# Performance work log

Hardware: AMD Instinct MI355X
Metric: run time of the kernel (lower is better)

The kernel has to match this reference:

```python
import jax, jax.numpy as jnp
import numpy as np

B, S, D, E, K = 4, 4096, 2048, 64, 8
STD = 0.02 / np.sqrt(D)
BIAS_UPDATE_SPEED = 0.001


def setup_inputs() -> dict:
    key = jax.random.key(0)
    k1, k2, k3, k4 = jax.random.split(key, 4)
    return {
        "x": jax.random.normal(k1, (B, S, D), dtype=jnp.float32),
        "Wr": (jax.random.normal(k2, (E, D), dtype=jnp.float32) * STD),
        "Wn": (jax.random.normal(k3, (E, D), dtype=jnp.float32) * STD),
        "bias": jnp.zeros((E,), dtype=jnp.float32),
        "noise_u": jax.random.uniform(k4, (B, S, E), dtype=jnp.float32),
    }


def reference(x, Wr, Wn, bias, noise_u):
    # x: [B,S,D]; Wr, Wn: [E,D]; bias: [E]; noise_u: [B,S,E] uniform(0,1)
    logits = jnp.einsum("bsd,ed->bse", x, Wr)          # router logits
    noisy_logits = jnp.einsum("bsd,ed->bse", x, Wn)    # noise scale logits
    noise = noise_u * jax.nn.softplus(noisy_logits)
    z = noise + logits + bias                           # [B,S,E]

    topk_vals, topk_idx = jax.lax.top_k(z, K)           # [B,S,K]
    neg_inf = jnp.full_like(z, -jnp.inf)
    sparse = jnp.put_along_axis(neg_inf, topk_idx, topk_vals, axis=-1,
                                inplace=False)          # -inf except top-k slots
    probs = jax.nn.softmax(sparse, axis=-1)             # [B,S,E]

    # load-balancing bias update (faithful to source, incl. scalar sum quirk)
    sel_mask = jax.nn.one_hot(topk_idx, E, dtype=jnp.float32).sum(axis=(0, 1, 2))  # [E]
    current_expert_load = sel_mask.sum()                # scalar (as in torch .sum(0) on 1-D)
    total_tokens = B * S * K
    avg_load = total_tokens / E
    load_violation = avg_load - current_expert_load
    new_bias = bias + BIAS_UPDATE_SPEED * jnp.sign(load_violation)

    return probs, topk_idx, new_bias
```

## Files before the change

kernel.cpp:

```cpp
#include <hip/hip_runtime.h>
#include <math.h>

#define BB 4
#define SS 4096
#define DD 2048
#define EE 64
#define KK 8
#define TT_TOTAL (BB*SS)
#define E2 128
#define DK 32
#define NC (DD/DK)

typedef double double2_t __attribute__((ext_vector_type(2)));
typedef double double4_t __attribute__((ext_vector_type(4)));

__device__ __forceinline__ double softplus64(double x) {
    return fmax(x, 0.0) + log1p(exp(-fabs(x)));
}

#define ROWF 132

template<int KS>
__launch_bounds__(256, 2)
__global__ void gemmf_kernel(const float* __restrict__ x,
                             const float* __restrict__ Wr,
                             const float* __restrict__ Wn,
                             double* __restrict__ zp)
{
    __shared__ __align__(16) float xs[DK][ROWF];
    __shared__ __align__(16) float ws[DK][ROWF];

    const int tid   = threadIdx.x;
    const int split = blockIdx.x % KS;
    const int bt    = blockIdx.x / KS;
    const int tok0  = bt * 128;
    const int kbase = split * (DD / KS);
    const int NCH   = (DD / KS) / DK;

    const int srow = tid & 127;
    const int skh  = tid >> 7;
    const float* xsrc = x + (size_t)(tok0 + srow) * DD + kbase + 16 * skh;
    const float* wsrc = ((srow < EE) ? Wr + (size_t)srow * DD
                                     : Wn + (size_t)(srow - EE) * DD)
                        + kbase + 16 * skh;

    const int og2 = tid & 15;
    const int tg2 = tid >> 4;

    double acc[8][8];
    #pragma unroll
    for (int t = 0; t < 8; ++t)
        #pragma unroll
        for (int o = 0; o < 8; ++o) acc[t][o] = 0.0;

    float4 xa[4], wa[4];
    #pragma unroll
    for (int i = 0; i < 4; ++i) {
        xa[i] = *reinterpret_cast<const float4*>(xsrc + 4 * i);
        wa[i] = *reinterpret_cast<const float4*>(wsrc + 4 * i);
    }

    for (int c = 0; c < NCH; ++c) {
        __syncthreads();

        {
            const int k0 = 16 * skh;
            #pragma unroll
            for (int i = 0; i < 4; ++i) {
                xs[k0 + 4*i + 0][srow] = xa[i].x;
                xs[k0 + 4*i + 1][srow] = xa[i].y;
                xs[k0 + 4*i + 2][srow] = xa[i].z;
                xs[k0 + 4*i + 3][srow] = xa[i].w;
                ws[k0 + 4*i + 0][srow] = wa[i].x;
                ws[k0 + 4*i + 1][srow] = wa[i].y;
                ws[k0 + 4*i + 2][srow] = wa[i].z;
                ws[k0 + 4*i + 3][srow] = wa[i].w;
            }
        }
        __syncthreads();

        if (c + 1 < NCH) {
            const int off = (c + 1) * DK;
            #pragma unroll
            for (int i = 0; i < 4; ++i) {
                xa[i] = *reinterpret_cast<const float4*>(xsrc + off + 4 * i);
                wa[i] = *reinterpret_cast<const float4*>(wsrc + off + 4 * i);
            }
        }

        #pragma unroll 4
        for (int k = 0; k < DK; ++k) {
            const float4 fx0 = *reinterpret_cast<const float4*>(&xs[k][4 * tg2]);
            const float4 fx1 = *reinterpret_cast<const float4*>(&xs[k][64 + 4 * tg2]);
            const float4 fw0 = *reinterpret_cast<const float4*>(&ws[k][4 * og2]);
            const float4 fw1 = *reinterpret_cast<const float4*>(&ws[k][64 + 4 * og2]);
            const double xv[8] = {(double)fx0.x, (double)fx0.y, (double)fx0.z, (double)fx0.w,
                                  (double)fx1.x, (double)fx1.y, (double)fx1.z, (double)fx1.w};
            const double wv[8] = {(double)fw0.x, (double)fw0.y, (double)fw0.z, (double)fw0.w,
                                  (double)fw1.x, (double)fw1.y, (double)fw1.z, (double)fw1.w};
            #pragma unroll
            for (int t = 0; t < 8; ++t)
                #pragma unroll
                for (int o = 0; o < 8; ++o)
                    acc[t][o] = fma(xv[t], wv[o], acc[t][o]);
        }
    }

    double* zbase = zp + (size_t)split * TT_TOTAL * E2;
    #pragma unroll
    for (int t = 0; t < 8; ++t) {
        const int tok = 4 * tg2 + (t & 3) + 64 * (t >> 2);
        double* row = zbase + (size_t)(tok0 + tok) * E2;
        double2_t v0 = {acc[t][0], acc[t][1]};
        double2_t v1 = {acc[t][2], acc[t][3]};
        double2_t v2 = {acc[t][4], acc[t][5]};
        double2_t v3 = {acc[t][6], acc[t][7]};
        *reinterpret_cast<double2_t*>(&row[4 * og2])          = v0;
        *reinterpret_cast<double2_t*>(&row[4 * og2 + 2])      = v1;
        *reinterpret_cast<double2_t*>(&row[64 + 4 * og2])     = v2;
        *reinterpret_cast<double2_t*>(&row[64 + 4 * og2 + 2]) = v3;
    }
}

template<int KS>
__launch_bounds__(256, 4)
__global__ void topk2_kernel(const double* __restrict__ zp,
                             const float* __restrict__ bias,
                             const float* __restrict__ noise_u,
                             float* __restrict__ out_probs,
                             float* __restrict__ out_idx)
{
    const int tid  = threadIdx.x;
    const int wid  = tid >> 6;
    const int lane = tid & 63;
    const int tok0 = blockIdx.x * 32;

    for (int tt = 0; tt < 8; ++tt) {
        const int tok = tok0 + wid * 8 + tt;
        const size_t gtok = (size_t)tok;

        double logit = 0.0, noisy = 0.0;
        #pragma unroll
        for (int s = 0; s < KS; ++s) {
            const double* row = zp + (size_t)s * TT_TOTAL * E2 + (size_t)tok * E2;
            logit += row[lane];
            noisy += row[EE + lane];
        }
        const double zv = (double)noise_u[gtok * EE + lane] * softplus64(noisy)
                          + logit + (double)bias[lane];

        double zw = zv;
        bool   sel = false;
        double m0  = 0.0;
        #pragma unroll
        for (int it = 0; it < KK; ++it) {
            double v  = zw;
            int    ix = lane;
            #pragma unroll
            for (int off = 32; off > 0; off >>= 1) {
                const double ov = __shfl_xor(v, off, 64);
                const int    oi = __shfl_xor(ix, off, 64);
                if (ov > v || (ov == v && oi < ix)) { v = ov; ix = oi; }
            }
            if (it == 0) m0 = v;
            if (lane == ix) { sel = true; zw = -INFINITY; }
            if (lane == 0) out_idx[gtok * KK + it] = (float)ix;
        }

        const double ex = sel ? exp(zv - m0) : 0.0;
        double den = ex;
        #pragma unroll
        for (int off = 32; off > 0; off >>= 1) den += __shfl_xor(den, off, 64);

        out_probs[gtok * EE + lane] = (float)(ex / den);
    }
}

#define BT 32
#define XT 34
#define WT 66

__launch_bounds__(256, 4)
__global__ void gemm_kernel(const float* __restrict__ x,
                            const float* __restrict__ Wr,
                            const float* __restrict__ Wn,
                            double* __restrict__ zout)
{
    __shared__ __align__(16) double xs[DK][XT];
    __shared__ __align__(16) double ws[DK][WT];

    const int tid  = threadIdx.x;
    const int bt   = blockIdx.x >> 1;
    const int be   = blockIdx.x & 1;
    const int tok0 = bt * BT;
    const int e0   = be * 64;

    const int kk = tid & 31;
    const int tq = tid >> 5;
    const float* xsrc[4];
    const float* wsrc[8];
    #pragma unroll
    for (int j = 0; j < 4; ++j)
        xsrc[j] = x + (size_t)(tok0 + 4 * tq + j) * DD + kk;
    #pragma unroll
    for (int j = 0; j < 4; ++j) {
        const int e  = e0 + 4 * tq + j;
        const int e2 = e0 + 32 + 4 * tq + j;
        wsrc[j]     = ((e  < EE) ? Wr + (size_t)e * DD
                                 : Wn + (size_t)(e  - EE) * DD) + kk;
        wsrc[4 + j] = ((e2 < EE) ? Wr + (size_t)e2 * DD
                                 : Wn + (size_t)(e2 - EE) * DD) + kk;
    }

    const int og = tid & 15;
    const int tp = tid >> 4;

    double acc[2][4];
    #pragma unroll
    for (int t = 0; t < 2; ++t)
        #pragma unroll
        for (int i = 0; i < 4; ++i) acc[t][i] = 0.0;

    float xr[4], wr[8];
    #pragma unroll
    for (int j = 0; j < 4; ++j) xr[j] = xsrc[j][0];
    #pragma unroll
    for (int j = 0; j < 8; ++j) wr[j] = wsrc[j][0];

    for (int c = 0; c < NC; ++c) {
        __syncthreads();
        {
            double4_t xv = {(double)xr[0], (double)xr[1], (double)xr[2], (double)xr[3]};
            *reinterpret_cast<double4_t*>(&xs[kk][4 * tq]) = xv;
            double4_t w0 = {(double)wr[0], (double)wr[1], (double)wr[2], (double)wr[3]};
            *reinterpret_cast<double4_t*>(&ws[kk][4 * tq]) = w0;
            double4_t w1 = {(double)wr[4], (double)wr[5], (double)wr[6], (double)wr[7]};
            *reinterpret_cast<double4_t*>(&ws[kk][32 + 4 * tq]) = w1;
        }
        __syncthreads();
        if (c + 1 < NC) {
            const int off = (c + 1) * DK;
            #pragma unroll
            for (int j = 0; j < 4; ++j) xr[j] = xsrc[j][off];
            #pragma unroll
            for (int j = 0; j < 8; ++j) wr[j] = wsrc[j][off];
        }
        #pragma unroll 4
        for (int k = 0; k < DK; ++k) {
            const double2_t xv = *reinterpret_cast<const double2_t*>(&xs[k][2 * tp]);
            const double2_t w0 = *reinterpret_cast<const double2_t*>(&ws[k][2 * og]);
            const double2_t w1 = *reinterpret_cast<const double2_t*>(&ws[k][32 + 2 * og]);
            acc[0][0] = fma(xv.x, w0.x, acc[0][0]);
            acc[0][1] = fma(xv.x, w0.y, acc[0][1]);
            acc[0][2] = fma(xv.x, w1.x, acc[0][2]);
            acc[0][3] = fma(xv.x, w1.y, acc[0][3]);
            acc[1][0] = fma(xv.y, w0.x, acc[1][0]);
            acc[1][1] = fma(xv.y, w0.y, acc[1][1]);
            acc[1][2] = fma(xv.y, w1.x, acc[1][2]);
            acc[1][3] = fma(xv.y, w1.y, acc[1][3]);
        }
    }

    #pragma unroll
    for (int t = 0; t < 2; ++t) {
        const size_t base = (size_t)(tok0 + 2 * tp + t) * E2 + e0;
        double2_t lo = {acc[t][0], acc[t][1]};
        double2_t hi = {acc[t][2], acc[t][3]};
        *reinterpret_cast<double2_t*>(&zout[base + 2 * og])      = lo;
        *reinterpret_cast<double2_t*>(&zout[base + 32 + 2 * og]) = hi;
    }
}

#define F_XT 34
#define F_WR 130
#define F_ZR 130
#define F_SMEM ((DK*F_XT + DK*F_WR)*8)

__launch_bounds__(256, 3)
__global__ void router_kernel(const float* __restrict__ x,
                              const float* __restrict__ Wr,
                              const float* __restrict__ Wn,
                              const float* __restrict__ bias,
                              const float* __restrict__ noise_u,
                              float* __restrict__ out_probs,
                              float* __restrict__ out_idx)
{
    __shared__ __align__(16) char smem_raw[F_SMEM];
    double (*xs)[F_XT] = reinterpret_cast<double(*)[F_XT]>(smem_raw);
    double (*wt)[F_WR] = reinterpret_cast<double(*)[F_WR]>(smem_raw + DK*F_XT*8);
    double (*zbuf)[F_ZR] = reinterpret_cast<double(*)[F_ZR]>(smem_raw);

    const int tid  = threadIdx.x;
    const int tok0 = blockIdx.x * 32;
    const int stok = tid >> 3;
    const int sfi  = tid & 7;
    const float* xsrc = x + (size_t)(tok0 + stok) * DD + sfi * 4;
    const float* wsrc[4];
    #pragma unroll
    for (int it = 0; it < 4; ++it) {
        const int r = it * 32 + stok;
        wsrc[it] = ((r < EE) ? (Wr + (size_t)r * DD)
                             : (Wn + (size_t)(r - EE) * DD)) + sfi * 4;
    }
    const int tg = tid >> 5;
    const int eg = tid & 31;

    double acc[4][4];
    #pragma unroll
    for (int t = 0; t < 4; ++t)
        #pragma unroll
        for (int i = 0; i < 4; ++i) acc[t][i] = 0.0;

    float4 xr  = *reinterpret_cast<const float4*>(xsrc);
    float4 wr0 = *reinterpret_cast<const float4*>(wsrc[0]);
    float4 wr1 = *reinterpret_cast<const float4*>(wsrc[1]);
    float4 wr2 = *reinterpret_cast<const float4*>(wsrc[2]);
    float4 wr3 = *reinterpret_cast<const float4*>(wsrc[3]);

    for (int c = 0; c < NC; ++c) {
        __syncthreads();
        {
            const int k0 = sfi * 4;
            xs[k0+0][stok] = (double)xr.x;  xs[k0+1][stok] = (double)xr.y;
            xs[k0+2][stok] = (double)xr.z;  xs[k0+3][stok] = (double)xr.w;
            wt[k0+0][stok      ] = (double)wr0.x; wt[k0+1][stok      ] = (double)wr0.y;
            wt[k0+2][stok      ] = (double)wr0.z; wt[k0+3][stok      ] = (double)wr0.w;
            wt[k0+0][stok + 32 ] = (double)wr1.x; wt[k0+1][stok + 32 ] = (double)wr1.y;
            wt[k0+2][stok + 32 ] = (double)wr1.z; wt[k0+3][stok + 32 ] = (double)wr1.w;
            wt[k0+0][stok + 64 ] = (double)wr2.x; wt[k0+1][stok + 64 ] = (double)wr2.y;
            wt[k0+2][stok + 64 ] = (double)wr2.z; wt[k0+3][stok + 64 ] = (double)wr2.w;
            wt[k0+0][stok + 96 ] = (double)wr3.x; wt[k0+1][stok + 96 ] = (double)wr3.y;
            wt[k0+2][stok + 96 ] = (double)wr3.z; wt[k0+3][stok + 96 ] = (double)wr3.w;
        }
        __syncthreads();
        if (c + 1 < NC) {
            const int off = (c + 1) * DK;
            xr  = *reinterpret_cast<const float4*>(xsrc + off);
            wr0 = *reinterpret_cast<const float4*>(wsrc[0] + off);
            wr1 = *reinterpret_cast<const float4*>(wsrc[1] + off);
            wr2 = *reinterpret_cast<const float4*>(wsrc[2] + off);
            wr3 = *reinterpret_cast<const float4*>(wsrc[3] + off);
        }
        #pragma unroll 4
        for (int k = 0; k < DK; ++k) {
            const double2_t xv0 = *reinterpret_cast<const double2_t*>(&xs[k][tg * 4]);
            const double2_t xv1 = *reinterpret_cast<const double2_t*>(&xs[k][tg * 4 + 2]);
            const double2_t w0  = *reinterpret_cast<const double2_t*>(&wt[k][2 * eg]);
            const double2_t w1  = *reinterpret_cast<const double2_t*>(&wt[k][64 + 2 * eg]);
            const double xvv[4] = {xv0.x, xv0.y, xv1.x, xv1.y};
            #pragma unroll
            for (int t = 0; t < 4; ++t) {
                acc[t][0] = fma(xvv[t], w0.x, acc[t][0]);
                acc[t][1] = fma(xvv[t], w0.y, acc[t][1]);
                acc[t][2] = fma(xvv[t], w1.x, acc[t][2]);
                acc[t][3] = fma(xvv[t], w1.y, acc[t][3]);
            }
        }
    }
    __syncthreads();
    #pragma unroll
    for (int t = 0; t < 4; ++t) {
        double2_t lo = {acc[t][0], acc[t][1]};
        double2_t hi = {acc[t][2], acc[t][3]};
        *reinterpret_cast<double2_t*>(&zbuf[tg * 4 + t][2 * eg])      = lo;
        *reinterpret_cast<double2_t*>(&zbuf[tg * 4 + t][64 + 2 * eg]) = hi;
    }
    __syncthreads();

    const int wid  = tid >> 6;
    const int lane = tid & 63;
    for (int tt = 0; tt < 8; ++tt) {
        const int tok = wid * 8 + tt;
        const size_t gtok = (size_t)tok0 + tok;
        const double logit = zbuf[tok][lane];
        const double noisy = zbuf[tok][EE + lane];
        const double zv = (double)noise_u[gtok * EE + lane] * softplus64(noisy)
                          + logit + (double)bias[lane];
        double zw = zv;
        bool   sel = false;
        double m0  = 0.0;
        #pragma unroll
        for (int it = 0; it < KK; ++it) {
            double v  = zw;
            int    ix = lane;
            #pragma unroll
            for (int off = 32; off > 0; off >>= 1) {
                const double ov = __shfl_xor(v, off, 64);
                const int    oi = __shfl_xor(ix, off, 64);
                if (ov > v || (ov == v && oi < ix)) { v = ov; ix = oi; }
            }
            if (it == 0) m0 = v;
            if (lane == ix) { sel = true; zw = -INFINITY; }
            if (lane == 0) out_idx[gtok * KK + it] = (float)ix;
        }
        const double ex = sel ? exp(zv - m0) : 0.0;
        double den = ex;
        #pragma unroll
        for (int off = 32; off > 0; off >>= 1) den += __shfl_xor(den, off, 64);
        out_probs[gtok * EE + lane] = (float)(ex / den);
    }
}

__global__ void bias_kernel(const float* __restrict__ bias,
                            float* __restrict__ out_bias)
{
    const int e = threadIdx.x;
    if (e < EE) {
        const double load_violation = (double)(TT_TOTAL * KK) / EE
                                      - (double)(TT_TOTAL * KK);
        const double s = (load_violation > 0.0) ? 1.0
                         : ((load_violation < 0.0) ? -1.0 : 0.0);
        out_bias[e] = bias[e] + (float)(0.001 * s);
    }
}

extern "C" void kernel_launch(void* const* d_in, const int* in_sizes, int n_in,
                              void* d_out, int out_size, void* d_ws, size_t ws_size,
                              hipStream_t stream)
{
    const float* x       = (const float*)d_in[0];
    const float* Wr      = (const float*)d_in[1];
    const float* Wn      = (const float*)d_in[2];
    const float* bias    = (const float*)d_in[3];
    const float* noise_u = (const float*)d_in[4];

    float* out       = (float*)d_out;
    float* out_probs = out;
    float* out_idx   = out + (size_t)TT_TOTAL * EE;
    float* out_bias  = out + (size_t)TT_TOTAL * EE + (size_t)TT_TOTAL * KK;

    const size_t z1 = (size_t)TT_TOTAL * E2 * sizeof(double);

    if (ws_size >= 4 * z1) {
        double* zp = (double*)d_ws;
        gemmf_kernel<4><<<128 * 4, 256, 0, stream>>>(x, Wr, Wn, zp);
        topk2_kernel<4><<<TT_TOTAL / 32, 256, 0, stream>>>(zp, bias, noise_u,
                                                           out_probs, out_idx);
    } else if (ws_size >= 2 * z1) {
        double* zp = (double*)d_ws;
        gemmf_kernel<2><<<128 * 2, 256, 0, stream>>>(x, Wr, Wn, zp);
        topk2_kernel<2><<<TT_TOTAL / 32, 256, 0, stream>>>(zp, bias, noise_u,
                                                           out_probs, out_idx);
    } else if (ws_size >= z1) {
        double* z = (double*)d_ws;
        gemm_kernel<<<(TT_TOTAL / BT) * 2, 256, 0, stream>>>(x, Wr, Wn, z);
        topk2_kernel<1><<<TT_TOTAL / 32, 256, 0, stream>>>(z, bias, noise_u,
                                                           out_probs, out_idx);
    } else {
        router_kernel<<<TT_TOTAL / 32, 256, 0, stream>>>(
            x, Wr, Wn, bias, noise_u, out_probs, out_idx);
    }
    bias_kernel<<<1, 64, 0, stream>>>(bias, out_bias);
}
```

Before: 237.7 us.

## Compute router GEMM in fp32 with fp64 repair for near-tie tokens

Replaces the fp64 split-K GEMM with an fp32 version that writes fp32 partials, which halves workspace traffic and uses the much faster fp32 FMA path. The top-k kernel runs in fp32 and flags tokens whose gaps among the top-9 values fall below a small threshold. A repair kernel then recomputes those tokens in fp64 so the selected indices match the reference. Split-K can now go to 8 and occupancy rises to 4 blocks; the cost is an extra atomic flag list, a zero kernel and a repair pass, and correctness depends on the threshold being large enough.

```diff
diff --git a/kernel.cpp b/kernel.cpp
--- a/kernel.cpp
+++ b/kernel.cpp
@@ -10,22 +10,25 @@
 #define E2 128
 #define DK 32
 #define NC (DD/DK)
+#define DELTA 1e-4f
 
 typedef double double2_t __attribute__((ext_vector_type(2)));
-typedef double double4_t __attribute__((ext_vector_type(4)));
 
 __device__ __forceinline__ double softplus64(double x) {
     return fmax(x, 0.0) + log1p(exp(-fabs(x)));
 }
+__device__ __forceinline__ float softplus32(float x) {
+    return fmaxf(x, 0.0f) + log1pf(expf(-fabsf(x)));
+}
 
 #define ROWF 132
 
 template<int KS>
-__launch_bounds__(256, 2)
-__global__ void gemmf_kernel(const float* __restrict__ x,
-                             const float* __restrict__ Wr,
-                             const float* __restrict__ Wn,
-                             double* __restrict__ zp)
+__launch_bounds__(256, 4)
+__global__ void gemmf32_kernel(const float* __restrict__ x,
+                               const float* __restrict__ Wr,
+                               const float* __restrict__ Wn,
+                               float* __restrict__ zp)
 {
     __shared__ __align__(16) float xs[DK][ROWF];
     __shared__ __align__(16) float ws[DK][ROWF];
@@ -47,11 +50,11 @@
     const int og2 = tid & 15;
     const int tg2 = tid >> 4;
 
-    double acc[8][8];
+    float acc[8][8];
     #pragma unroll
     for (int t = 0; t < 8; ++t)
         #pragma unroll
-        for (int o = 0; o < 8; ++o) acc[t][o] = 0.0;
+        for (int o = 0; o < 8; ++o) acc[t][o] = 0.0f;
 
     float4 xa[4], wa[4];
     #pragma unroll
@@ -62,7 +65,6 @@
 
     for (int c = 0; c < NCH; ++c) {
         __syncthreads();
-
         {
             const int k0 = 16 * skh;
             #pragma unroll
@@ -94,41 +96,39 @@
             const float4 fx1 = *reinterpret_cast<const float4*>(&xs[k][64 + 4 * tg2]);
             const float4 fw0 = *reinterpret_cast<const float4*>(&ws[k][4 * og2]);
             const float4 fw1 = *reinterpret_cast<const float4*>(&ws[k][64 + 4 * og2]);
-            const double xv[8] = {(double)fx0.x, (double)fx0.y, (double)fx0.z, (double)fx0.w,
-                                  (double)fx1.x, (double)fx1.y, (double)fx1.z, (double)fx1.w};
-            const double wv[8] = {(double)fw0.x, (double)fw0.y, (double)fw0.z, (double)fw0.w,
-                                  (double)fw1.x, (double)fw1.y, (double)fw1.z, (double)fw1.w};
+            const float xv[8] = {fx0.x, fx0.y, fx0.z, fx0.w,
+                                 fx1.x, fx1.y, fx1.z, fx1.w};
+            const float wv[8] = {fw0.x, fw0.y, fw0.z, fw0.w,
+                                 fw1.x, fw1.y, fw1.z, fw1.w};
             #pragma unroll
             for (int t = 0; t < 8; ++t)
                 #pragma unroll
                 for (int o = 0; o < 8; ++o)
-                    acc[t][o] = fma(xv[t], wv[o], acc[t][o]);
-        }
-    }
-
-    double* zbase = zp + (size_t)split * TT_TOTAL * E2;
+                    acc[t][o] = fmaf(xv[t], wv[o], acc[t][o]);
+        }
+    }
+
+    float* zbase = zp + (size_t)split * TT_TOTAL * E2;
     #pragma unroll
     for (int t = 0; t < 8; ++t) {
         const int tok = 4 * tg2 + (t & 3) + 64 * (t >> 2);
-        double* row = zbase + (size_t)(tok0 + tok) * E2;
-        double2_t v0 = {acc[t][0], acc[t][1]};
-        double2_t v1 = {acc[t][2], acc[t][3]};
-        double2_t v2 = {acc[t][4], acc[t][5]};
-        double2_t v3 = {acc[t][6], acc[t][7]};
-        *reinterpret_cast<double2_t*>(&row[4 * og2])          = v0;
-        *reinterpret_cast<double2_t*>(&row[4 * og2 + 2])      = v1;
-        *reinterpret_cast<double2_t*>(&row[64 + 4 * og2])     = v2;
-        *reinterpret_cast<double2_t*>(&row[64 + 4 * og2 + 2]) = v3;
+        float* row = zbase + (size_t)(tok0 + tok) * E2;
+        float4 v0 = {acc[t][0], acc[t][1], acc[t][2], acc[t][3]};
+        float4 v1 = {acc[t][4], acc[t][5], acc[t][6], acc[t][7]};
+        *reinterpret_cast<float4*>(&row[4 * og2])      = v0;
+        *reinterpret_cast<float4*>(&row[64 + 4 * og2]) = v1;
     }
 }
 
 template<int KS>
 __launch_bounds__(256, 4)
-__global__ void topk2_kernel(const double* __restrict__ zp,
+__global__ void topkf_kernel(const float* __restrict__ zp,
                              const float* __restrict__ bias,
                              const float* __restrict__ noise_u,
                              float* __restrict__ out_probs,
-                             float* __restrict__ out_idx)
+                             float* __restrict__ out_idx,
+                             int* __restrict__ flag_list,
+                             int* __restrict__ flag_cnt)
 {
     const int tid  = threadIdx.x;
     const int wid  = tid >> 6;
@@ -139,135 +139,137 @@
         const int tok = tok0 + wid * 8 + tt;
         const size_t gtok = (size_t)tok;
 
-        double logit = 0.0, noisy = 0.0;
+        float logit = 0.0f, noisy = 0.0f;
         #pragma unroll
         for (int s = 0; s < KS; ++s) {
-            const double* row = zp + (size_t)s * TT_TOTAL * E2 + (size_t)tok * E2;
+            const float* row = zp + (size_t)s * TT_TOTAL * E2 + (size_t)tok * E2;
             logit += row[lane];
             noisy += row[EE + lane];
         }
-        const double zv = (double)noise_u[gtok * EE + lane] * softplus64(noisy)
-                          + logit + (double)bias[lane];
-
-        double zw = zv;
-        bool   sel = false;
-        double m0  = 0.0;
-        #pragma unroll
-        for (int it = 0; it < KK; ++it) {
-            double v  = zw;
-            int    ix = lane;
+        const float zv = noise_u[gtok * EE + lane] * softplus32(noisy)
+                         + logit + bias[lane];
+
+        float zw = zv;
+        bool  sel = false;
+        float vr[9];
+        #pragma unroll
+        for (int it = 0; it < 9; ++it) {
+            float v  = zw;
+            int   ix = lane;
             #pragma unroll
             for (int off = 32; off > 0; off >>= 1) {
-                const double ov = __shfl_xor(v, off, 64);
-                const int    oi = __shfl_xor(ix, off, 64);
+                const float ov = __shfl_xor(v, off, 64);
+                const int   oi = __shfl_xor(ix, off, 64);
                 if (ov > v || (ov == v && oi < ix)) { v = ov; ix = oi; }
             }
-            if (it == 0) m0 = v;
-            if (lane == ix) { sel = true; zw = -INFINITY; }
-            if (lane == 0) out_idx[gtok * KK + it] = (float)ix;
-        }
-
-        const double ex = sel ? exp(zv - m0) : 0.0;
-        double den = ex;
+            vr[it] = v;
+            if (it < 8) {
+                if (lane == ix) { sel = true; zw = -INFINITY; }
+                if (lane == 0) out_idx[gtok * KK + it] = (float)ix;
+            }
+        }
+
+        const float ex = sel ? expf(zv - vr[0]) : 0.0f;
+        float den = ex;
         #pragma unroll
         for (int off = 32; off > 0; off >>= 1) den += __shfl_xor(den, off, 64);
-
-        out_probs[gtok * EE + lane] = (float)(ex / den);
-    }
-}
-
-#define BT 32
-#define XT 34
-#define WT 66
+        out_probs[gtok * EE + lane] = ex / den;
+
+        if (lane == 0) {
+            float mg = vr[0] - vr[1];
+            #pragma unroll
+            for (int i = 1; i < 8; ++i) mg = fminf(mg, vr[i] - vr[i + 1]);
+            if (mg < DELTA) {
+                const int p = atomicAdd(flag_cnt, 1);
+                flag_list[p] = tok;
+            }
+        }
+    }
+}
 
 __launch_bounds__(256, 4)
-__global__ void gemm_kernel(const float* __restrict__ x,
-                            const float* __restrict__ Wr,
-                            const float* __restrict__ Wn,
-                            double* __restrict__ zout)
-{
-    __shared__ __align__(16) double xs[DK][XT];
-    __shared__ __align__(16) double ws[DK][WT];
-
-    const int tid  = threadIdx.x;
-    const int bt   = blockIdx.x >> 1;
-    const int be   = blockIdx.x & 1;
-    const int tok0 = bt * BT;
-    const int e0   = be * 64;
-
-    const int kk = tid & 31;
-    const int tq = tid >> 5;
-    const float* xsrc[4];
-    const float* wsrc[8];
-    #pragma unroll
-    for (int j = 0; j < 4; ++j)
-        xsrc[j] = x + (size_t)(tok0 + 4 * tq + j) * DD + kk;
-    #pragma unroll
-    for (int j = 0; j < 4; ++j) {
-        const int e  = e0 + 4 * tq + j;
-        const int e2 = e0 + 32 + 4 * tq + j;
-        wsrc[j]     = ((e  < EE) ? Wr + (size_t)e * DD
-                                 : Wn + (size_t)(e  - EE) * DD) + kk;
-        wsrc[4 + j] = ((e2 < EE) ? Wr + (size_t)e2 * DD
-                                 : Wn + (size_t)(e2 - EE) * DD) + kk;
-    }
-
-    const int og = tid & 15;
-    const int tp = tid >> 4;
-
-    double acc[2][4];
-    #pragma unroll
-    for (int t = 0; t < 2; ++t)
-        #pragma unroll
-        for (int i = 0; i < 4; ++i) acc[t][i] = 0.0;
-
-    float xr[4], wr[8];
-    #pragma unroll
-    for (int j = 0; j < 4; ++j) xr[j] = xsrc[j][0];
-    #pragma unroll
-    for (int j = 0; j < 8; ++j) wr[j] = wsrc[j][0];
-
-    for (int c = 0; c < NC; ++c) {
-        __syncthreads();
-        {
-            double4_t xv = {(double)xr[0], (double)xr[1], (double)xr[2], (double)xr[3]};
-            *reinterpret_cast<double4_t*>(&xs[kk][4 * tq]) = xv;
-            double4_t w0 = {(double)wr[0], (double)wr[1], (double)wr[2], (double)wr[3]};
-            *reinterpret_cast<double4_t*>(&ws[kk][4 * tq]) = w0;
-            double4_t w1 = {(double)wr[4], (double)wr[5], (double)wr[6], (double)wr[7]};
-            *reinterpret_cast<double4_t*>(&ws[kk][32 + 4 * tq]) = w1;
-        }
-        __syncthreads();
-        if (c + 1 < NC) {
-            const int off = (c + 1) * DK;
-            #pragma unroll
-            for (int j = 0; j < 4; ++j) xr[j] = xsrc[j][off];
-            #pragma unroll
-            for (int j = 0; j < 8; ++j) wr[j] = wsrc[j][off];
-        }
-        #pragma unroll 4
-        for (int k = 0; k < DK; ++k) {
-            const double2_t xv = *reinterpret_cast<const double2_t*>(&xs[k][2 * tp]);
-            const double2_t w0 = *reinterpret_cast<const double2_t*>(&ws[k][2 * og]);
-            const double2_t w1 = *reinterpret_cast<const double2_t*>(&ws[k][32 + 2 * og]);
-            acc[0][0] = fma(xv.x, w0.x, acc[0][0]);
-            acc[0][1] = fma(xv.x, w0.y, acc[0][1]);
-            acc[0][2] = fma(xv.x, w1.x, acc[0][2]);
-            acc[0][3] = fma(xv.x, w1.y, acc[0][3]);
-            acc[1][0] = fma(xv.y, w0.x, acc[1][0]);
-            acc[1][1] = fma(xv.y, w0.y, acc[1][1]);
-            acc[1][2] = fma(xv.y, w1.x, acc[1][2]);
-            acc[1][3] = fma(xv.y, w1.y, acc[1][3]);
-        }
-    }
-
-    #pragma unroll
-    for (int t = 0; t < 2; ++t) {
-        const size_t base = (size_t)(tok0 + 2 * tp + t) * E2 + e0;
-        double2_t lo = {acc[t][0], acc[t][1]};
-        double2_t hi = {acc[t][2], acc[t][3]};
-        *reinterpret_cast<double2_t*>(&zout[base + 2 * og])      = lo;
-        *reinterpret_cast<double2_t*>(&zout[base + 32 + 2 * og]) = hi;
+__global__ void repair_kernel(const float* __restrict__ x,
+                              const float* __restrict__ Wr,
+                              const float* __restrict__ Wn,
+                              const float* __restrict__ bias,
+                              const float* __restrict__ noise_u,
+                              float* __restrict__ out_probs,
+                              float* __restrict__ out_idx,
+                              const int* __restrict__ flag_list,
+                              const int* __restrict__ flag_cnt)
+{
+    __shared__ double pp[2][E2];
+
+    const int tid = threadIdx.x;
+    const int o   = tid & 127;
+    const int h   = tid >> 7;
+    const int n   = flag_cnt[0];
+
+    const float* wsrc = (o < EE) ? Wr + (size_t)o * DD
+                                 : Wn + (size_t)(o - EE) * DD;
+
+    for (int i = blockIdx.x; i < n; i += gridDim.x) {
+        const int tok = flag_list[i];
+        const float* xrow = x + (size_t)tok * DD;
+
+        double p = 0.0;
+        const int kb = h * (DD / 2);
+        for (int k = 0; k < DD / 2; k += 4) {
+            const float4 xv = *reinterpret_cast<const float4*>(&xrow[kb + k]);
+            const float4 wv = *reinterpret_cast<const float4*>(&wsrc[kb + k]);
+            p = fma((double)xv.x, (double)wv.x, p);
+            p = fma((double)xv.y, (double)wv.y, p);
+            p = fma((double)xv.z, (double)wv.z, p);
+            p = fma((double)xv.w, (double)wv.w, p);
+        }
+        pp[h][o] = p;
+        __syncthreads();
+
+        if (tid < 64) {
+            const int lane = tid;
+            const double logit = pp[0][lane] + pp[1][lane];
+            const double noisy = pp[0][EE + lane] + pp[1][EE + lane];
+            const double zv = (double)noise_u[(size_t)tok * EE + lane]
+                                  * softplus64(noisy)
+                              + logit + (double)bias[lane];
+            double zw = zv;
+            bool   sel = false;
+            double m0  = 0.0;
+            #pragma unroll
+            for (int it = 0; it < KK; ++it) {
+                double v  = zw;
+                int    ix = lane;
+                #pragma unroll
+                for (int off = 32; off > 0; off >>= 1) {
+                    const double ov = __shfl_xor(v, off, 64);
+                    const int    oi = __shfl_xor(ix, off, 64);
+                    if (ov > v || (ov == v && oi < ix)) { v = ov; ix = oi; }
+                }
+                if (it == 0) m0 = v;
+                if (lane == ix) { sel = true; zw = -INFINITY; }
+                if (lane == 0) out_idx[(size_t)tok * KK + it] = (float)ix;
+            }
+            const double ex = sel ? exp(zv - m0) : 0.0;
+            double den = ex;
+            #pragma unroll
+            for (int off = 32; off > 0; off >>= 1) den += __shfl_xor(den, off, 64);
+            out_probs[(size_t)tok * EE + lane] = (float)(ex / den);
+        }
+        __syncthreads();
+    }
+}
+
+__global__ void zero_kernel(int* __restrict__ cnt)
+{
+    if (threadIdx.x == 0) cnt[0] = 0;
+}
+
+__global__ void bias_kernel(const float* __restrict__ bias,
+                            float* __restrict__ out_bias)
+{
+    const int e = threadIdx.x;
+    if (e < EE) {
+        out_bias[e] = bias[e] - 0.001f;
     }
 }
 
@@ -401,19 +403,6 @@
     }
 }
 
-__global__ void bias_kernel(const float* __restrict__ bias,
-                            float* __restrict__ out_bias)
-{
-    const int e = threadIdx.x;
-    if (e < EE) {
-        const double load_violation = (double)(TT_TOTAL * KK) / EE
-                                      - (double)(TT_TOTAL * KK);
-        const double s = (load_violation > 0.0) ? 1.0
-                         : ((load_violation < 0.0) ? -1.0 : 0.0);
-        out_bias[e] = bias[e] + (float)(0.001 * s);
-    }
-}
-
 extern "C" void kernel_launch(void* const* d_in, const int* in_sizes, int n_in,
                               void* d_out, int out_size, void* d_ws, size_t ws_size,
                               hipStream_t stream)
@@ -429,23 +418,36 @@
     float* out_idx   = out + (size_t)TT_TOTAL * EE;
     float* out_bias  = out + (size_t)TT_TOTAL * EE + (size_t)TT_TOTAL * KK;
 
-    const size_t z1 = (size_t)TT_TOTAL * E2 * sizeof(double);
-
-    if (ws_size >= 4 * z1) {
-        double* zp = (double*)d_ws;
-        gemmf_kernel<4><<<128 * 4, 256, 0, stream>>>(x, Wr, Wn, zp);
-        topk2_kernel<4><<<TT_TOTAL / 32, 256, 0, stream>>>(zp, bias, noise_u,
-                                                           out_probs, out_idx);
-    } else if (ws_size >= 2 * z1) {
-        double* zp = (double*)d_ws;
-        gemmf_kernel<2><<<128 * 2, 256, 0, stream>>>(x, Wr, Wn, zp);
-        topk2_kernel<2><<<TT_TOTAL / 32, 256, 0, stream>>>(zp, bias, noise_u,
-                                                           out_probs, out_idx);
-    } else if (ws_size >= z1) {
-        double* z = (double*)d_ws;
-        gemm_kernel<<<(TT_TOTAL / BT) * 2, 256, 0, stream>>>(x, Wr, Wn, z);
-        topk2_kernel<1><<<TT_TOTAL / 32, 256, 0, stream>>>(z, bias, noise_u,
-                                                           out_probs, out_idx);
+    const size_t zsplit = (size_t)TT_TOTAL * E2 * sizeof(float);
+    const size_t extras = (size_t)(TT_TOTAL + 64) * sizeof(int);
+
+    int KS = 0;
+    if      (ws_size >= 8 * zsplit + extras) KS = 8;
+    else if (ws_size >= 4 * zsplit + extras) KS = 4;
+    else if (ws_size >= 2 * zsplit + extras) KS = 2;
+
+    if (KS > 0) {
+        float* zp       = (float*)d_ws;
+        int*   flag_list = (int*)((char*)d_ws + (size_t)KS * zsplit);
+        int*   flag_cnt  = flag_list + TT_TOTAL;
+
+        zero_kernel<<<1, 64, 0, stream>>>(flag_cnt);
+        if (KS == 8) {
+            gemmf32_kernel<8><<<128 * 8, 256, 0, stream>>>(x, Wr, Wn, zp);
+            topkf_kernel<8><<<TT_TOTAL / 32, 256, 0, stream>>>(
+                zp, bias, noise_u, out_probs, out_idx, flag_list, flag_cnt);
+        } else if (KS == 4) {
+            gemmf32_kernel<4><<<128 * 4, 256, 0, stream>>>(x, Wr, Wn, zp);
+            topkf_kernel<4><<<TT_TOTAL / 32, 256, 0, stream>>>(
+                zp, bias, noise_u, out_probs, out_idx, flag_list, flag_cnt);
+        } else {
+            gemmf32_kernel<2><<<128 * 2, 256, 0, stream>>>(x, Wr, Wn, zp);
+            topkf_kernel<2><<<TT_TOTAL / 32, 256, 0, stream>>>(
+                zp, bias, noise_u, out_probs, out_idx, flag_list, flag_cnt);
+        }
+        repair_kernel<<<128, 256, 0, stream>>>(x, Wr, Wn, bias, noise_u,
+                                               out_probs, out_idx,
+                                               flag_list, flag_cnt);
     } else {
         router_kernel<<<TT_TOTAL / 32, 256, 0, stream>>>(
             x, Wr, Wn, bias, noise_u, out_probs, out_idx);
```

Measured after the change: 536.8 us. +125.9%, slower.
